# Kernel tuning notes

Measured on AMD Instinct MI355X. Metric: run time of the kernel, lower is better.

## Reference

```python
import jax, jax.numpy as jnp
import numpy as np

EPS = 1e-05  # norm_epsilon

def setup_inputs() -> dict:
    key = jax.random.key(0)
    ks = jax.random.split(key, 6)
    B, T, D, E, N, C = 16, 512, 256, 16, 8192, 1
    xs = jax.random.normal(ks[0], (B, T, D), jnp.float32)
    pad_mask = jnp.ones((B, T), dtype=bool)
    masked_masks = jax.random.randint(ks[1], (B, T), 0, 2) > 0
    ln_gamma = jnp.ones((D,), jnp.float32)
    ln_beta = jnp.zeros((D,), jnp.float32)
    # xavier_normal init for the (frozen) random projection
    projection = jax.random.normal(ks[2], (D, E), jnp.float32) * (2.0 / (D + E)) ** 0.5
    embeddings = jax.random.normal(ks[3], (C, E, N), jnp.float32)
    top_n_out = jax.random.normal(ks[4], (C, D, N), jnp.float32) * 0.02
    mask_emb = jax.random.normal(ks[5], (D,), jnp.float32) * 0.1
    return {"xs": xs, "pad_mask": pad_mask, "masked_masks": masked_masks,
            "ln_gamma": ln_gamma, "ln_beta": ln_beta, "projection": projection,
            "embeddings": embeddings, "top_n_out": top_n_out, "mask_emb": mask_emb}

def reference(xs, pad_mask, masked_masks, ln_gamma, ln_beta, projection, embeddings, top_n_out, mask_emb):
    B, T, D = xs.shape
    C = embeddings.shape[0]
    # ---- target path: layer norm -> random projection -> nearest codebook idx ----
    mu = jnp.mean(xs, -1, keepdims=True)
    var = jnp.mean((xs - mu) ** 2, -1, keepdims=True)
    h = (xs - mu) / jnp.sqrt(var + EPS) * ln_gamma + ln_beta
    proj = jnp.einsum('btd,de->bte', h, projection).reshape(B * T, -1)  # [BT,E]
    # pairwise squared distances: [C, BT, N]
    dist = (jnp.sum(proj ** 2, axis=1)[None, :, None]
            + jnp.sum(embeddings ** 2, axis=1)[:, None, :]
            - 2.0 * jnp.einsum('te,cen->ctn', proj, embeddings))
    target = jnp.argmin(dist, axis=-1).T.reshape(B, T, C)  # [B,T,C] int
    # ---- masked input -> encoder (identity stand-in) -> per-codebook logits ----
    masked_xs = jnp.where(masked_masks[..., None], mask_emb, xs)
    logits = jnp.einsum('btd,cdn->btcn', masked_xs, top_n_out)  # [B,T,C,N]
    logp = jax.nn.log_softmax(logits, axis=-1)
    ce = -jnp.take_along_axis(logp, target[..., None], axis=-1)[..., 0]  # [B,T,C]
    m = (pad_mask & masked_masks).astype(logits.dtype)  # [B,T]
    loss = jnp.sum(ce * m[..., None]) / (jnp.sum(m) * C)
    return loss
```

## Files before the change

### kernel.cpp

```cpp
#include <hip/hip_runtime.h>
#include <hip/hip_bf16.h>
#include <math.h>

#define BT   8192
#define DD   256
#define EE   16
#define NN   8192

typedef __attribute__((ext_vector_type(8))) short short8;
typedef __attribute__((ext_vector_type(4))) float f32x4;

__device__ __forceinline__ unsigned short f2bf(float x) {
  union { float f; unsigned int u; } c; c.f = x;
  unsigned int r = (c.u + 0x7FFFu + ((c.u >> 16) & 1u)) >> 16;
  return (unsigned short)r;
}
__device__ __forceinline__ unsigned int ordf(float d) {
  union { float f; unsigned int u; } c; c.f = d;
  return ((int)c.u < 0) ? ~c.u : (c.u | 0x80000000u);
}
__device__ __forceinline__ unsigned long long shflxor64(unsigned long long v, int m) {
  unsigned int lo = (unsigned int)v, hi = (unsigned int)(v >> 32);
  lo = __shfl_xor((int)lo, m);
  hi = __shfl_xor((int)hi, m);
  return ((unsigned long long)hi << 32) | lo;
}
__device__ __forceinline__ void gload_lds16(const void* g, void* l) {
  __builtin_amdgcn_global_load_lds((const __attribute__((address_space(1))) void*)g,
                                   (__attribute__((address_space(3))) void*)l, 16, 0, 0);
}

#define XT_LD 65
__global__ __launch_bounds__(256) void k_pre(const float* __restrict__ xs,
                                             const int* __restrict__ mm,
                                             const float* __restrict__ memb,
                                             const float* __restrict__ gamma,
                                             const float* __restrict__ beta,
                                             const float* __restrict__ P,
                                             const float* __restrict__ W,
                                             const float* __restrict__ emb,
                                             unsigned short* __restrict__ xmb,
                                             unsigned short* __restrict__ projb,
                                             unsigned short* __restrict__ Wt,
                                             unsigned short* __restrict__ embT,
                                             float* __restrict__ sqe,
                                             unsigned long long* __restrict__ keys,
                                             float* __restrict__ sumexp) {
  __shared__ __align__(16) float xt[32 * XT_LD * 4];
  __shared__ float stats[32][2];
  int bid = blockIdx.x;
  int tid = threadIdx.x;

  if (bid < 512) {
    int n0 = (bid & 127) * 64;
    int d0 = (bid >> 7) * 64;
    #pragma unroll
    for (int pass = 0; pass < 16; pass++) {
      int idx = pass * 256 + tid;
      int dd = idx >> 6, ln = idx & 63;
      xt[ln * 65 + dd] = W[(size_t)(d0 + dd) * NN + n0 + ln];
    }
    __syncthreads();
    #pragma unroll
    for (int pass = 0; pass < 2; pass++) {
      int g = pass * 256 + tid;
      int row = g >> 3, c8 = g & 7;
      short8 v;
      #pragma unroll
      for (int i = 0; i < 8; i++) v[i] = (short)f2bf(xt[row * 65 + c8 * 8 + i]);
      *(short8*)(Wt + (size_t)(n0 + row) * DD + d0 + c8 * 8) = v;
    }
    return;
  }
  if (bid < 544) {
    int n = (bid - 512) * 256 + tid;
    float e[EE];
    float sq = 0.f;
    #pragma unroll
    for (int k = 0; k < EE; k++) { e[k] = emb[k * NN + n]; sq += e[k] * e[k]; }
    short8 lo, hi;
    #pragma unroll
    for (int k = 0; k < 8; k++) { lo[k] = (short)f2bf(e[k]); hi[k] = (short)f2bf(e[k + 8]); }
    *(short8*)(embT + (size_t)n * EE)     = lo;
    *(short8*)(embT + (size_t)n * EE + 8) = hi;
    sqe[n] = sq;
    keys[n] = ~0ULL;
    return;
  }
  int pb = bid - 544;
  int t0 = pb * 32;
  int w = tid >> 6;
  int col4 = tid & 63;
  float4 mb4 = ((const float4*)memb)[col4];

  #pragma unroll
  for (int j = 0; j < 8; j++) {
    int k = tid + j * 256;
    int row = w + j * 4;
    float4 xv = ((const float4*)xs)[(size_t)pb * 2048 + k];
    int m = mm[t0 + row];
    float4 v = m ? mb4 : xv;
    ushort2 o01 = { f2bf(v.x), f2bf(v.y) };
    ushort2 o23 = { f2bf(v.z), f2bf(v.w) };
    ((ushort2*)(xmb + (size_t)(t0 + row) * DD + col4 * 4))[0] = o01;
    ((ushort2*)(xmb + (size_t)(t0 + row) * DD + col4 * 4))[1] = o23;
    *(float4*)&xt[(row * XT_LD + col4) * 4] = xv;
  }
  __syncthreads();
  {
    int t = tid >> 3, g = tid & 7;
    float s = 0.f, s2 = 0.f;
    #pragma unroll
    for (int i = 0; i < 8; i++) {
      float4 v = *(const float4*)&xt[(t * XT_LD + g * 8 + i) * 4];
      s  += v.x + v.y + v.z + v.w;
      s2 += v.x * v.x + v.y * v.y + v.z * v.z + v.w * v.w;
    }
    #pragma unroll
    for (int m = 1; m <= 4; m <<= 1) { s += __shfl_xor(s, m); s2 += __shfl_xor(s2, m); }
    if (g == 0) {
      float mu = s * (1.0f / DD);
      float var = s2 * (1.0f / DD) - mu * mu;
      stats[t][0] = mu;
      stats[t][1] = rsqrtf(var + 1e-5f);
    }
  }
  if (tid < 32) sumexp[t0 + tid] = 0.f;
  __syncthreads();
  {
    int t = tid >> 3, e0 = (tid & 7) * 2;
    float mu = stats[t][0], rstd = stats[t][1];
    float a0 = 0.f, a1 = 0.f;
    for (int d = 0; d < DD; d += 4) {
      float4 xv = *(const float4*)&xt[(t * XT_LD + (d >> 2)) * 4];
      float xd[4] = { xv.x, xv.y, xv.z, xv.w };
      #pragma unroll
      for (int dd = 0; dd < 4; dd++) {
        float h = (xd[dd] - mu) * rstd * gamma[d + dd] + beta[d + dd];
        a0 += h * P[(d + dd) * EE + e0];
        a1 += h * P[(d + dd) * EE + e0 + 1];
      }
    }
    ushort2 o = { f2bf(a0), f2bf(a1) };
    *(ushort2*)(projb + (size_t)(t0 + t) * EE + e0) = o;
  }
}

#define NS4 8
#define ASEG (NN / NS4)
__global__ __launch_bounds__(256) void k_argmin(const unsigned short* __restrict__ projb,
                                                const unsigned short* __restrict__ embT,
                                                const float* __restrict__ sqe,
                                                unsigned long long* __restrict__ keys) {
  int tid = threadIdx.x;
  int w = tid >> 6, lane = tid & 63;
  int q = lane >> 4, c = lane & 15;
  int tw = blockIdx.x * 64 + w * 16;
  int nseg = blockIdx.y * ASEG;

  short8 a = {0, 0, 0, 0, 0, 0, 0, 0};
  if (q < 2) a = *(const short8*)(projb + (size_t)(tw + c) * EE + q * 8);

  unsigned long long bk[4];
  #pragma unroll
  for (int r = 0; r < 4; r++) bk[r] = ~0ULL;

  #pragma unroll 2
  for (int it = 0; it < ASEG / 16; it++) {
    int n = nseg + it * 16 + c;
    short8 b = {0, 0, 0, 0, 0, 0, 0, 0};
    if (q < 2) b = *(const short8*)(embT + (size_t)n * EE + q * 8);
    float sq = sqe[n];
    f32x4 acc = (f32x4){0.f, 0.f, 0.f, 0.f};
    acc = __builtin_amdgcn_mfma_f32_16x16x32_bf16(a, b, acc, 0, 0, 0);
    #pragma unroll
    for (int r = 0; r < 4; r++) {
      float dist = sq - 2.f * acc[r];
      unsigned long long key = ((unsigned long long)ordf(dist) << 32) | (unsigned int)n;
      bk[r] = key < bk[r] ? key : bk[r];
    }
  }
  #pragma unroll
  for (int r = 0; r < 4; r++) {
    #pragma unroll
    for (int m = 1; m <= 8; m <<= 1) {
      unsigned long long o = shflxor64(bk[r], m);
      bk[r] = o < bk[r] ? o : bk[r];
    }
  }
  if (c == 0) {
    #pragma unroll
    for (int r = 0; r < 4; r++)
      atomicMin(&keys[tw + q * 4 + r], bk[r]);
  }
}

__global__ __launch_bounds__(512, 4) void k_ce5(const unsigned short* __restrict__ xmb,
                                                const unsigned short* __restrict__ Wt,
                                                const unsigned long long* __restrict__ keys,
                                                float* __restrict__ sumexp,
                                                float* __restrict__ ltar) {
  __shared__ __align__(16) unsigned short ldsA[3][128 * 32];
  __shared__ __align__(16) unsigned short ldsB[3][128 * 32];
  int tid = threadIdx.x;
  int lane = tid & 63;
  int w = tid >> 6;
  int q = lane >> 4, c = lane & 15;
  int wm = w >> 1, wn = w & 1;
  int t0 = blockIdx.x * 128;
  int n0 = blockIdx.y * 128;
  int sw = q ^ ((c >> 1) & 3);

  f32x4 acc[2][4];
  #pragma unroll
  for (int mi = 0; mi < 2; mi++)
    #pragma unroll
    for (int ni = 0; ni < 4; ni++) acc[mi][ni] = (f32x4){0.f, 0.f, 0.f, 0.f};

  #define STAGE(buf, itv) do {                                                  \
    int kk_ = (itv) * 32;                                                       \
    int g = tid;                                                                \
    int row = g >> 2;                                                           \
    int qg = (g & 3) ^ ((g >> 3) & 3);                                          \
    gload_lds16(xmb + (size_t)(t0 + row) * DD + kk_ + qg * 8,                   \
                ldsA[buf] + g * 8);                                             \
    gload_lds16(Wt + (size_t)(n0 + row) * DD + kk_ + qg * 8,                    \
                ldsB[buf] + g * 8);                                             \
  } while (0)

  STAGE(0, 0);
  STAGE(1, 1);
  asm volatile("s_waitcnt vmcnt(2)" ::: "memory");
  __builtin_amdgcn_s_barrier();

  #pragma unroll
  for (int it = 0; it < 8; it++) {
    const int cur = it % 3;
    const int nxt = (it + 2) % 3;
    if (it + 2 < 8) {
      if (nxt == 0)      STAGE(0, it + 2);
      else if (nxt == 1) STAGE(1, it + 2);
      else               STAGE(2, it + 2);
    }

    short8 a[2], b[4];
    #pragma unroll
    for (int mi = 0; mi < 2; mi++)
      a[mi] = *(const short8*)(ldsA[cur] + (wm * 32 + mi * 16 + c) * 32 + sw * 8);
    #pragma unroll
    for (int ni = 0; ni < 4; ni++)
      b[ni] = *(const short8*)(ldsB[cur] + (wn * 64 + ni * 16 + c) * 32 + sw * 8);
    #pragma unroll
    for (int mi = 0; mi < 2; mi++)
      #pragma unroll
      for (int ni = 0; ni < 4; ni++)
        acc[mi][ni] = __builtin_amdgcn_mfma_f32_16x16x32_bf16(a[mi], b[ni], acc[mi][ni], 0, 0, 0);

    if (it < 6) {
      asm volatile("s_waitcnt vmcnt(2)" ::: "memory");
      __builtin_amdgcn_s_barrier();
    } else if (it == 6) {
      asm volatile("s_waitcnt vmcnt(0)" ::: "memory");
      __builtin_amdgcn_s_barrier();
    }
  }
  #undef STAGE

  int tg[2][4];
  #pragma unroll
  for (int mi = 0; mi < 2; mi++)
    #pragma unroll
    for (int r = 0; r < 4; r++)
      tg[mi][r] = (int)(unsigned int)(keys[t0 + wm * 32 + mi * 16 + q * 4 + r] & 0xFFFFFFFFULL);

  float rs[2][4];
  #pragma unroll
  for (int mi = 0; mi < 2; mi++)
    #pragma unroll
    for (int r = 0; r < 4; r++) rs[mi][r] = 0.f;

  #pragma unroll
  for (int mi = 0; mi < 2; mi++)
    #pragma unroll
    for (int ni = 0; ni < 4; ni++) {
      int col = n0 + wn * 64 + ni * 16 + c;
      #pragma unroll
      for (int r = 0; r < 4; r++) {
        float v = acc[mi][ni][r];
        if (col == tg[mi][r])
          ltar[t0 + wm * 32 + mi * 16 + q * 4 + r] = v;
        rs[mi][r] += __expf(v);
      }
    }

  #pragma unroll
  for (int mi = 0; mi < 2; mi++)
    #pragma unroll
    for (int r = 0; r < 4; r++) {
      float s = rs[mi][r];
      s += __shfl_xor(s, 1);
      s += __shfl_xor(s, 2);
      s += __shfl_xor(s, 4);
      s += __shfl_xor(s, 8);
      if (c == 0)
        atomicAdd(&sumexp[t0 + wm * 32 + mi * 16 + q * 4 + r], s);
    }
}

__global__ __launch_bounds__(1024) void k_final(const float* __restrict__ sumexp,
                                                const float* __restrict__ ltar,
                                                const int* __restrict__ padm,
                                                const int* __restrict__ mm,
                                                float* __restrict__ out) {
  int tid = threadIdx.x;
  float sum = 0.f, cnt = 0.f;
  for (int t = tid; t < BT; t += 1024) {
    float ce = __logf(sumexp[t]) - ltar[t];
    if (padm[t] && mm[t]) { sum += ce; cnt += 1.f; }
  }
  #pragma unroll
  for (int off = 32; off; off >>= 1) { sum += __shfl_down(sum, off); cnt += __shfl_down(cnt, off); }
  __shared__ float rs[16], rc[16];
  int wid = tid >> 6, lane = tid & 63;
  if (lane == 0) { rs[wid] = sum; rc[wid] = cnt; }
  __syncthreads();
  if (tid == 0) {
    float S = 0.f, Cn = 0.f;
    for (int i = 0; i < 16; i++) { S += rs[i]; Cn += rc[i]; }
    out[0] = S / Cn;
  }
}

extern "C" void kernel_launch(void* const* d_in, const int* in_sizes, int n_in,
                              void* d_out, int out_size, void* d_ws, size_t ws_size,
                              hipStream_t stream) {
  const float* xs    = (const float*)d_in[0];
  const int*   padm  = (const int*)d_in[1];
  const int*   mm    = (const int*)d_in[2];
  const float* gamma = (const float*)d_in[3];
  const float* beta  = (const float*)d_in[4];
  const float* P     = (const float*)d_in[5];
  const float* emb   = (const float*)d_in[6];
  const float* W     = (const float*)d_in[7];
  const float* memb  = (const float*)d_in[8];
  float* out = (float*)d_out;

  char* ws = (char*)d_ws;
  size_t off = 0;
  unsigned short* xmb   = (unsigned short*)(ws + off); off += (size_t)BT * DD * 2;
  unsigned short* Wtb   = (unsigned short*)(ws + off); off += (size_t)NN * DD * 2;
  unsigned short* embT  = (unsigned short*)(ws + off); off += (size_t)NN * EE * 2;
  unsigned short* projb = (unsigned short*)(ws + off); off += (size_t)BT * EE * 2;
  float* sqe            = (float*)(ws + off);          off += (size_t)NN * 4;
  unsigned long long* keys = (unsigned long long*)(ws + off); off += (size_t)BT * 8;
  float* sumexp         = (float*)(ws + off);          off += (size_t)BT * 4;
  float* ltar           = (float*)(ws + off);          off += (size_t)BT * 4;

  k_pre   <<<800, 256, 0, stream>>>(xs, mm, memb, gamma, beta, P, W, emb,
                                    xmb, projb, Wtb, embT, sqe, keys, sumexp);
  k_argmin<<<dim3(BT / 64, NS4), 256, 0, stream>>>(projb, embT, sqe, keys);
  k_ce5   <<<dim3(64, 64), 512, 0, stream>>>(xmb, Wtb, keys, sumexp, ltar);
  k_final <<<1, 1024, 0, stream>>>(sumexp, ltar, padm, mm, out);
}
```

Baseline: 175.4 us.

## Fold final reduction into CE kernel via last-block pattern, stage projection params in LDS

```diff
diff --git a/kernel.cpp b/kernel.cpp
--- a/kernel.cpp
+++ b/kernel.cpp
@@ -45,9 +45,12 @@
                                              unsigned short* __restrict__ embT,
                                              float* __restrict__ sqe,
                                              unsigned long long* __restrict__ keys,
-                                             float* __restrict__ sumexp) {
+                                             float* __restrict__ sumexp,
+                                             int* __restrict__ done) {
   __shared__ __align__(16) float xt[32 * XT_LD * 4];
   __shared__ float stats[32][2];
+  __shared__ __align__(16) float Pl[DD * EE];
+  __shared__ __align__(16) float gl[DD], bl[DD];
   int bid = blockIdx.x;
   int tid = threadIdx.x;
 
@@ -73,6 +76,7 @@
     return;
   }
   if (bid < 544) {
+    if (bid == 512 && tid == 0) done[0] = 0;
     int n = (bid - 512) * 256 + tid;
     float e[EE];
     float sq = 0.f;
@@ -83,7 +87,7 @@
     for (int k = 0; k < 8; k++) { lo[k] = (short)f2bf(e[k]); hi[k] = (short)f2bf(e[k + 8]); }
     *(short8*)(embT + (size_t)n * EE)     = lo;
     *(short8*)(embT + (size_t)n * EE + 8) = hi;
-    sqe[n] = sq;
+    sqe[n] = 0.5f * sq;
     keys[n] = ~0ULL;
     return;
   }
@@ -92,6 +96,14 @@
   int w = tid >> 6;
   int col4 = tid & 63;
   float4 mb4 = ((const float4*)memb)[col4];
+
+  #pragma unroll
+  for (int i = tid; i < DD * EE / 4; i += 256)
+    ((float4*)Pl)[i] = ((const float4*)P)[i];
+  if (tid < DD / 4) {
+    ((float4*)gl)[tid] = ((const float4*)gamma)[tid];
+    ((float4*)bl)[tid] = ((const float4*)beta)[tid];
+  }
 
   #pragma unroll
   for (int j = 0; j < 8; j++) {
@@ -136,9 +148,9 @@
       float xd[4] = { xv.x, xv.y, xv.z, xv.w };
       #pragma unroll
       for (int dd = 0; dd < 4; dd++) {
-        float h = (xd[dd] - mu) * rstd * gamma[d + dd] + beta[d + dd];
-        a0 += h * P[(d + dd) * EE + e0];
-        a1 += h * P[(d + dd) * EE + e0 + 1];
+        float h = (xd[dd] - mu) * rstd * gl[d + dd] + bl[d + dd];
+        a0 += h * Pl[(d + dd) * EE + e0];
+        a1 += h * Pl[(d + dd) * EE + e0 + 1];
       }
     }
     ushort2 o = { f2bf(a0), f2bf(a1) };
@@ -161,25 +173,29 @@
   short8 a = {0, 0, 0, 0, 0, 0, 0, 0};
   if (q < 2) a = *(const short8*)(projb + (size_t)(tw + c) * EE + q * 8);
 
-  unsigned long long bk[4];
-  #pragma unroll
-  for (int r = 0; r < 4; r++) bk[r] = ~0ULL;
+  unsigned int bo[4], bi[4];
+  #pragma unroll
+  for (int r = 0; r < 4; r++) { bo[r] = 0xFFFFFFFFu; bi[r] = 0u; }
 
   #pragma unroll 2
   for (int it = 0; it < ASEG / 16; it++) {
     int n = nseg + it * 16 + c;
     short8 b = {0, 0, 0, 0, 0, 0, 0, 0};
     if (q < 2) b = *(const short8*)(embT + (size_t)n * EE + q * 8);
-    float sq = sqe[n];
+    float sqh = sqe[n];
     f32x4 acc = (f32x4){0.f, 0.f, 0.f, 0.f};
     acc = __builtin_amdgcn_mfma_f32_16x16x32_bf16(a, b, acc, 0, 0, 0);
     #pragma unroll
     for (int r = 0; r < 4; r++) {
-      float dist = sq - 2.f * acc[r];
-      unsigned long long key = ((unsigned long long)ordf(dist) << 32) | (unsigned int)n;
-      bk[r] = key < bk[r] ? key : bk[r];
-    }
-  }
+      float dist = sqh - acc[r];
+      unsigned int u = ordf(dist);
+      if (u < bo[r]) { bo[r] = u; bi[r] = (unsigned int)n; }
+    }
+  }
+  unsigned long long bk[4];
+  #pragma unroll
+  for (int r = 0; r < 4; r++)
+    bk[r] = ((unsigned long long)bo[r] << 32) | bi[r];
   #pragma unroll
   for (int r = 0; r < 4; r++) {
     #pragma unroll
@@ -199,7 +215,11 @@
                                                 const unsigned short* __restrict__ Wt,
                                                 const unsigned long long* __restrict__ keys,
                                                 float* __restrict__ sumexp,
-                                                float* __restrict__ ltar) {
+                                                float* __restrict__ ltar,
+                                                const int* __restrict__ padm,
+                                                const int* __restrict__ mm,
+                                                int* __restrict__ done,
+                                                float* __restrict__ out) {
   __shared__ __align__(16) unsigned short ldsA[3][128 * 32];
   __shared__ __align__(16) unsigned short ldsB[3][128 * 32];
   int tid = threadIdx.x;
@@ -250,11 +270,13 @@
     #pragma unroll
     for (int ni = 0; ni < 4; ni++)
       b[ni] = *(const short8*)(ldsB[cur] + (wn * 64 + ni * 16 + c) * 32 + sw * 8);
+    __builtin_amdgcn_s_setprio(1);
     #pragma unroll
     for (int mi = 0; mi < 2; mi++)
       #pragma unroll
       for (int ni = 0; ni < 4; ni++)
         acc[mi][ni] = __builtin_amdgcn_mfma_f32_16x16x32_bf16(a[mi], b[ni], acc[mi][ni], 0, 0, 0);
+    __builtin_amdgcn_s_setprio(0);
 
     if (it < 6) {
       asm volatile("s_waitcnt vmcnt(2)" ::: "memory");
@@ -305,28 +327,35 @@
       if (c == 0)
         atomicAdd(&sumexp[t0 + wm * 32 + mi * 16 + q * 4 + r], s);
     }
-}
-
-__global__ __launch_bounds__(1024) void k_final(const float* __restrict__ sumexp,
-                                                const float* __restrict__ ltar,
-                                                const int* __restrict__ padm,
-                                                const int* __restrict__ mm,
-                                                float* __restrict__ out) {
-  int tid = threadIdx.x;
-  float sum = 0.f, cnt = 0.f;
-  for (int t = tid; t < BT; t += 1024) {
-    float ce = __logf(sumexp[t]) - ltar[t];
-    if (padm[t] && mm[t]) { sum += ce; cnt += 1.f; }
-  }
-  #pragma unroll
-  for (int off = 32; off; off >>= 1) { sum += __shfl_down(sum, off); cnt += __shfl_down(cnt, off); }
-  __shared__ float rs[16], rc[16];
-  int wid = tid >> 6, lane = tid & 63;
-  if (lane == 0) { rs[wid] = sum; rc[wid] = cnt; }
+
+  __threadfence();
+  __shared__ int lastFlag;
+  if (tid == 0) {
+    int prev = atomicAdd(done, 1);
+    lastFlag = (prev == (int)(gridDim.x * gridDim.y) - 1);
+  }
+  __syncthreads();
+  if (!lastFlag) return;
+  __threadfence();
+  float fsum = 0.f, fcnt = 0.f;
+  for (int t = tid; t < BT; t += 512) {
+    float se = __hip_atomic_load(&sumexp[t], __ATOMIC_RELAXED, __HIP_MEMORY_SCOPE_AGENT);
+    float lt = __hip_atomic_load(&ltar[t], __ATOMIC_RELAXED, __HIP_MEMORY_SCOPE_AGENT);
+    float ce = __logf(se) - lt;
+    if (padm[t] && mm[t]) { fsum += ce; fcnt += 1.f; }
+  }
+  #pragma unroll
+  for (int off = 32; off; off >>= 1) {
+    fsum += __shfl_down(fsum, off);
+    fcnt += __shfl_down(fcnt, off);
+  }
+  __shared__ float frs[8], frc[8];
+  if (lane == 0) { frs[w] = fsum; frc[w] = fcnt; }
   __syncthreads();
   if (tid == 0) {
     float S = 0.f, Cn = 0.f;
-    for (int i = 0; i < 16; i++) { S += rs[i]; Cn += rc[i]; }
+    #pragma unroll
+    for (int i = 0; i < 8; i++) { S += frs[i]; Cn += frc[i]; }
     out[0] = S / Cn;
   }
 }
@@ -355,10 +384,11 @@
   unsigned long long* keys = (unsigned long long*)(ws + off); off += (size_t)BT * 8;
   float* sumexp         = (float*)(ws + off);          off += (size_t)BT * 4;
   float* ltar           = (float*)(ws + off);          off += (size_t)BT * 4;
+  int* done             = (int*)(ws + off);            off += 64;
 
   k_pre   <<<800, 256, 0, stream>>>(xs, mm, memb, gamma, beta, P, W, emb,
-                                    xmb, projb, Wtb, embT, sqe, keys, sumexp);
+                                    xmb, projb, Wtb, embT, sqe, keys, sumexp, done);
   k_argmin<<<dim3(BT / 64, NS4), 256, 0, stream>>>(projb, embT, sqe, keys);
-  k_ce5   <<<dim3(64, 64), 512, 0, stream>>>(xmb, Wtb, keys, sumexp, ltar);
-  k_final <<<1, 1024, 0, stream>>>(sumexp, ltar, padm, mm, out);
-}
+  k_ce5   <<<dim3(64, 64), 512, 0, stream>>>(xmb, Wtb, keys, sumexp, ltar,
+                                             padm, mm, done, out);
+}
```

Result: slower. 640.6 us (+265.1%).
